# Performance work log

Measured on AMD Instinct MI355X. Metric: run time of the kernel, lower is better.

Reference implementation:

```python
import jax, jax.numpy as jnp
import numpy as np

H = 8  # num_heads

def layernorm(x, g, b, eps=1e-5):
    mu = jnp.mean(x, axis=-1, keepdims=True)
    var = jnp.var(x, axis=-1, keepdims=True)
    return (x - mu) * jax.lax.rsqrt(var + eps) * g + b

def mha(x, w_in, b_in, w_out, b_out, bias=None):
    # x: [B_, S, D]; w_in: [3D, D] packed q,k,v (PyTorch MHA layout)
    B_, S, D = x.shape
    hd = D // H
    qkv = x @ w_in.T + b_in                      # [B_, S, 3D]
    q, k, v = jnp.split(qkv, 3, axis=-1)
    def heads(t):
        return t.reshape(B_, S, H, hd).transpose(0, 2, 1, 3)  # [B_, H, S, hd]
    q, k, v = heads(q), heads(k), heads(v)
    scores = jnp.einsum('bhqd,bhkd->bhqk', q, k) / jnp.sqrt(jnp.float32(hd))
    if bias is not None:
        scores = scores + bias[None, None]        # broadcast [S,S] bias
    attn = jax.nn.softmax(scores, axis=-1)
    out = jnp.einsum('bhqk,bhkd->bhqd', attn, v)  # [B_, H, S, hd]
    out = out.transpose(0, 2, 1, 3).reshape(B_, S, D)
    return out @ w_out.T + b_out

def setup_inputs() -> dict:
    key = jax.random.key(0)
    ks = jax.random.split(key, 8)
    B, T, N, D, F = 32, 12, 325, 128, 512
    s = 0.05
    return {
        'x': jax.random.normal(ks[0], (B, T, N, D), jnp.float32),
        't_w_in': jax.random.normal(ks[1], (3 * D, D), jnp.float32) * s,
        't_b_in': jnp.zeros((3 * D,), jnp.float32),
        't_w_out': jax.random.normal(ks[2], (D, D), jnp.float32) * s,
        't_b_out': jnp.zeros((D,), jnp.float32),
        's_w_in': jax.random.normal(ks[3], (3 * D, D), jnp.float32) * s,
        's_b_in': jnp.zeros((3 * D,), jnp.float32),
        's_w_out': jax.random.normal(ks[4], (D, D), jnp.float32) * s,
        's_b_out': jnp.zeros((D,), jnp.float32),
        'g_bias': jax.random.normal(ks[5], (N, N), jnp.float32) * 0.5,
        'norm_t_g': jnp.ones((D,), jnp.float32),
        'norm_t_b': jnp.zeros((D,), jnp.float32),
        'norm_s_g': jnp.ones((D,), jnp.float32),
        'norm_s_b': jnp.zeros((D,), jnp.float32),
        'ff_w1': jax.random.normal(ks[6], (F, D), jnp.float32) * s,
        'ff_b1': jnp.zeros((F,), jnp.float32),
        'ff_w2': jax.random.normal(ks[7], (D, F), jnp.float32) * s,
        'ff_b2': jnp.zeros((D,), jnp.float32),
        'norm_ff_g': jnp.ones((D,), jnp.float32),
        'norm_ff_b': jnp.zeros((D,), jnp.float32),
    }

def reference(x, t_w_in, t_b_in, t_w_out, t_b_out, s_w_in, s_b_in, s_w_out, s_b_out,
              g_bias, norm_t_g, norm_t_b, norm_s_g, norm_s_b,
              ff_w1, ff_b1, ff_w2, ff_b2, norm_ff_g, norm_ff_b):
    B, T, N, D = x.shape
    # Temporal attention: each sensor attends over time
    xt = x.transpose(0, 2, 1, 3).reshape(B * N, T, D)
    xt = mha(xt, t_w_in, t_b_in, t_w_out, t_b_out)
    x = layernorm(x + xt.reshape(B, N, T, D).transpose(0, 2, 1, 3), norm_t_g, norm_t_b)
    # Spatial attention with graph bias: each timestep attends over sensors
    xs = x.reshape(B * T, N, D)
    xs = mha(xs, s_w_in, s_b_in, s_w_out, s_b_out, bias=g_bias)
    x = layernorm(x + xs.reshape(B, T, N, D), norm_s_g, norm_s_b)
    # FFN
    h = jax.nn.gelu(x @ ff_w1.T + ff_b1) @ ff_w2.T + ff_b2
    x = layernorm(x + h, norm_ff_g, norm_ff_b)
    return x
```

## Files before the change

kernel.cpp:

```cpp
#include <hip/hip_runtime.h>
#include <cstdint>
#include <cstddef>


#define B_ 32
#define T_ 12
#define N_ 325
#define D_ 128
#define H_ 8
#define F_ 512
#define NT 124800
#define BCH 8
#define CHK (BCH * T_ * N_)
#define NCHUNK 4
#define GT ((CHK + 63) / 64)
#define NKT 11
#define NQT 21
#define QSPLIT 3
#define QPG 7
#define GBS 328

#define O_XBF 0UL
#define O_Y1B 31948800UL
#define O_QKV 63897600UL
#define O_ABUF 87859200UL
#define O_WB 95846400UL
#define O_PB 96370688UL

typedef __attribute__((ext_vector_type(8))) short bf16x8;
typedef __attribute__((ext_vector_type(4))) short bf16x4;
typedef __attribute__((ext_vector_type(4))) float f32x4;

__device__ inline float b2f(unsigned short b) {
  unsigned int u = ((unsigned int)b) << 16;
  return __builtin_bit_cast(float, u);
}
__device__ inline unsigned short f2b(float f) {
  unsigned int u = __builtin_bit_cast(unsigned int, f);
  unsigned int r = (u + 0x7FFFu + ((u >> 16) & 1u)) >> 16;
  return (unsigned short)r;
}
__device__ inline unsigned short f2b_fast(float f) {
  unsigned int u = __builtin_bit_cast(unsigned int, f);
  return (unsigned short)((u + 0x8000u) >> 16);
}
__device__ inline f32x4 mfma16(bf16x8 a, bf16x8 b, f32x4 c) {
  return __builtin_amdgcn_mfma_f32_16x16x32_bf16(a, b, c, 0, 0, 0);
}
#if __has_builtin(__builtin_amdgcn_mfma_f32_16x16x16bf16_1k)
__device__ inline f32x4 mfma16k16(bf16x4 a, bf16x4 b, f32x4 c) {
  return __builtin_amdgcn_mfma_f32_16x16x16bf16_1k(a, b, c, 0, 0, 0);
}
#else
__device__ inline f32x4 mfma16k16(bf16x4 a, bf16x4 b, f32x4 c) {
  f32x4 d;
  asm volatile("s_nop 3\n\t"
               "v_mfma_f32_16x16x16_bf16 %0, %1, %2, %3\n\t"
               "s_nop 7\n\ts_nop 7"
               : "=&v"(d)
               : "v"(a), "v"(b), "v"(c));
  return d;
}
#endif
__device__ inline float gelu_t(float x) {
  float x3 = x * x * x;
  return 0.5f * x * (1.0f + tanhf(0.7978845608f * (x + 0.044715f * x3)));
}

__global__ void k_convert8(const void* __restrict__ src,
                           unsigned short* __restrict__ dB, long n8,
                           const unsigned short* __restrict__ probe) {
  long i = (long)blockIdx.x * blockDim.x + threadIdx.x;
  if (i >= n8) return;
  if (probe[0] != 0) {
    ((uint4*)dB)[i] = ((const uint4*)src)[i];
  } else {
    float4 a = ((const float4*)src)[i * 2];
    float4 b = ((const float4*)src)[i * 2 + 1];
    uint4 o;
    unsigned short* op = (unsigned short*)&o;
    op[0] = f2b(a.x); op[1] = f2b(a.y); op[2] = f2b(a.z); op[3] = f2b(a.w);
    op[4] = f2b(b.x); op[5] = f2b(b.y); op[6] = f2b(b.z); op[7] = f2b(b.w);
    ((uint4*)dB)[i] = o;
  }
}

__global__ void k_conv_params(
    const void* s1, const void* s2, const void* s3, const void* s4,
    const void* s5, const void* s6, const void* s7, const void* s8,
    const void* s9, const void* s10, const void* s11, const void* s12,
    const void* s13, const void* s14, const void* s15, const void* s16,
    const void* s17, const void* s18, const void* s19, char* ws,
    const unsigned short* __restrict__ probe) {
  long i = (long)blockIdx.x * blockDim.x + threadIdx.x;
  bool isbf = probe[0] != 0;
  long o = 0;
#define LOADV(src, j) \
  (isbf ? b2f(((const unsigned short*)(src))[j]) : ((const float*)(src))[j])
#define SEGB(src, dstoff, n)                                        \
  if (i < o + (n)) {                                                \
    long j = i - o;                                                 \
    ((unsigned short*)(ws + (dstoff)))[j] = f2b(LOADV(src, j));     \
    return;                                                         \
  }                                                                 \
  o += (n);
#define SEGF(src, dstoff, n)                              \
  if (i < o + (n)) {                                      \
    long j = i - o;                                       \
    ((float*)(ws + (dstoff)))[j] = LOADV(src, j);         \
    return;                                               \
  }                                                       \
  o += (n);
  SEGB(s1, O_WB + 0, 49152)
  SEGF(s2, O_PB + 0, 384)
  SEGB(s3, O_WB + 98304, 16384)
  SEGF(s4, O_PB + 1536, 128)
  SEGB(s5, O_WB + 131072, 49152)
  SEGF(s6, O_PB + 2048, 384)
  SEGB(s7, O_WB + 229376, 16384)
  SEGF(s8, O_PB + 3584, 128)
  if (i < o + 326 * GBS) {
    long j = i - o;
    int q = (int)(j / GBS);
    int s = (int)(j - (long)q * GBS);
    float v = (q < 325 && s < 325) ? LOADV(s9, (long)q * 325 + s) : 0.0f;
    ((float*)(ws + O_PB + 9728))[j] = v;
    return;
  }
  o += 326 * GBS;
  SEGF(s10, O_PB + 6656, 128)
  SEGF(s11, O_PB + 7168, 128)
  SEGF(s12, O_PB + 7680, 128)
  SEGF(s13, O_PB + 8192, 128)
  SEGB(s14, O_WB + 262144, 65536)
  SEGF(s15, O_PB + 4096, 512)
  SEGB(s16, O_WB + 393216, 65536)
  SEGF(s17, O_PB + 6144, 128)
  SEGF(s18, O_PB + 8704, 128)
  SEGF(s19, O_PB + 9216, 128)
#undef SEGB
#undef SEGF
#undef LOADV
}
#define CONVP_TOTAL 371504L

template <int ROWS, int KTOT>
__device__ inline void stage_tile(short (*dst)[ROWS][32],
                                  const unsigned short* __restrict__ src,
                                  int row0, int k0, int tid, int Mrows) {
  constexpr int CH = ROWS * 16;
#pragma unroll
  for (int it = 0; it < CH / 256; ++it) {
    int cb = tid + it * 256;
    int row = cb >> 4;
    int kc = cb & 15;
    int gr = row0 + row;
    gr = gr < Mrows ? gr : Mrows - 1;
    uint4 v = *(const uint4*)(src + (size_t)gr * KTOT + (size_t)k0 + kc * 8);
    *(uint4*)(&dst[kc >> 2][row][(kc & 3) * 8]) = v;
  }
}

template <int KTOT, bool GELU>
__global__ __launch_bounds__(256) void k_gemm_store(
    const unsigned short* __restrict__ Ab, const unsigned short* __restrict__ Wb,
    const float* __restrict__ bias, unsigned short* __restrict__ outB, int Ntot,
    int Mrows, int Nrows) {
  __shared__ __align__(16) union USm {
    struct { short A[4][64][32]; short B[4][64][32]; } s;
    float C[64][68];
  } sm;
  const int tid = threadIdx.x;
  const int m0 = blockIdx.x * 64;
  const int n0 = blockIdx.y * 64;
  const int lane = tid & 63, wave = tid >> 6;
  const int wm = wave >> 1, wn = wave & 1;
  const int ml = lane & 15, quad = lane >> 4;
  f32x4 acc[2][2] = {};
#pragma unroll
  for (int c = 0; c < KTOT / 128; ++c) {
    if (c) __syncthreads();
    stage_tile<64, KTOT>(sm.s.A, Ab, m0, c * 128, tid, Mrows);
    stage_tile<64, KTOT>(sm.s.B, Wb, n0, c * 128, tid, Nrows);
    __syncthreads();
#pragma unroll
    for (int kc = 0; kc < 4; ++kc) {
      bf16x8 a0 = *(const bf16x8*)&sm.s.A[kc][wm * 32 + ml][quad * 8];
      bf16x8 a1 = *(const bf16x8*)&sm.s.A[kc][wm * 32 + 16 + ml][quad * 8];
      bf16x8 b0 = *(const bf16x8*)&sm.s.B[kc][wn * 32 + ml][quad * 8];
      bf16x8 b1 = *(const bf16x8*)&sm.s.B[kc][wn * 32 + 16 + ml][quad * 8];
      acc[0][0] = mfma16(a0, b0, acc[0][0]);
      acc[0][1] = mfma16(a0, b1, acc[0][1]);
      acc[1][0] = mfma16(a1, b0, acc[1][0]);
      acc[1][1] = mfma16(a1, b1, acc[1][1]);
    }
  }
  __syncthreads();
#pragma unroll
  for (int mi = 0; mi < 2; ++mi)
#pragma unroll
    for (int ni = 0; ni < 2; ++ni)
#pragma unroll
      for (int r = 0; r < 4; ++r)
        sm.C[wm * 32 + mi * 16 + quad * 4 + r][wn * 32 + ni * 16 + ml] =
            acc[mi][ni][r];
  __syncthreads();
  const int trow = tid >> 4;
  const int tcol = (tid & 15) * 4;
  const float4 bv = *(const float4*)&bias[n0 + tcol];
#pragma unroll
  for (int it = 0; it < 4; ++it) {
    int row = it * 16 + trow;
    int gm = m0 + row;
    float4 cv = *(const float4*)&sm.C[row][tcol];
    float v0 = cv.x + bv.x, v1 = cv.y + bv.y, v2 = cv.z + bv.z,
          v3 = cv.w + bv.w;
    if (GELU) {
      v0 = gelu_t(v0); v1 = gelu_t(v1); v2 = gelu_t(v2); v3 = gelu_t(v3);
    }
    if (gm < Mrows) {
      ushort4 ov;
      ov.x = f2b(v0); ov.y = f2b(v1); ov.z = f2b(v2); ov.w = f2b(v3);
      *(ushort4*)&outB[(size_t)gm * Ntot + n0 + tcol] = ov;
    }
  }
}

template <int KTOT, bool FINAL>
__global__ __launch_bounds__(256) void k_gemm_ln(
    const unsigned short* __restrict__ Ab, const unsigned short* __restrict__ Wb,
    const float* __restrict__ bias, const unsigned short* __restrict__ resid,
    const float* __restrict__ gamma, const float* __restrict__ beta,
    unsigned short* __restrict__ outB, void* __restrict__ dOut, size_t row0g,
    const unsigned short* __restrict__ probe, int Mrows) {
  __shared__ __align__(16) union USm {
    struct { short A[4][64][32]; short B[4][128][32]; } s;
    float C[64][132];
  } sm;
  const int tid = threadIdx.x;
  const int m0 = blockIdx.x * 64;
  const int lane = tid & 63, wave = tid >> 6;
  const int wm = wave >> 1, wn = wave & 1;
  const int ml = lane & 15, quad = lane >> 4;
  f32x4 acc[2][4] = {};
#pragma unroll
  for (int c = 0; c < KTOT / 128; ++c) {
    if (c) __syncthreads();
    stage_tile<64, KTOT>(sm.s.A, Ab, m0, c * 128, tid, Mrows);
    stage_tile<128, KTOT>(sm.s.B, Wb, 0, c * 128, tid, 128);
    __syncthreads();
#pragma unroll
    for (int kc = 0; kc < 4; ++kc) {
      bf16x8 a[2], b[4];
#pragma unroll
      for (int mi = 0; mi < 2; ++mi)
        a[mi] = *(const bf16x8*)&sm.s.A[kc][wm * 32 + mi * 16 + ml][quad * 8];
#pragma unroll
      for (int ni = 0; ni < 4; ++ni)
        b[ni] = *(const bf16x8*)&sm.s.B[kc][wn * 64 + ni * 16 + ml][quad * 8];
#pragma unroll
      for (int mi = 0; mi < 2; ++mi)
#pragma unroll
        for (int ni = 0; ni < 4; ++ni)
          acc[mi][ni] = mfma16(a[mi], b[ni], acc[mi][ni]);
    }
  }
  __syncthreads();
#pragma unroll
  for (int mi = 0; mi < 2; ++mi)
#pragma unroll
    for (int ni = 0; ni < 4; ++ni)
#pragma unroll
      for (int r = 0; r < 4; ++r)
        sm.C[wm * 32 + mi * 16 + quad * 4 + r][wn * 64 + ni * 16 + ml] =
            acc[mi][ni][r];
  __syncthreads();
  const int c0 = lane * 2;
  const float bia0 = bias[c0], bia1 = bias[c0 + 1];
  const float ga0 = gamma[c0], ga1 = gamma[c0 + 1];
  const float be0 = beta[c0], be1 = beta[c0 + 1];
  const bool isbf = FINAL ? (probe[0] != 0) : true;
#pragma unroll
  for (int rr = 0; rr < 16; ++rr) {
    int row = wave * 16 + rr;
    int gm = m0 + row;
    bool valid = gm < Mrows;
    float2 cc = *(const float2*)&sm.C[row][c0];
    float r0 = 0.f, r1 = 0.f;
    if (valid) {
      ushort2 rv = *(const ushort2*)&resid[(size_t)gm * 128 + c0];
      r0 = b2f(rv.x);
      r1 = b2f(rv.y);
    }
    float v0 = cc.x + bia0 + r0, v1 = cc.y + bia1 + r1;
    float s = v0 + v1, q = v0 * v0 + v1 * v1;
#pragma unroll
    for (int off = 1; off < 64; off <<= 1) {
      s += __shfl_xor(s, off);
      q += __shfl_xor(q, off);
    }
    float mean = s * (1.f / 128.f);
    float var = q * (1.f / 128.f) - mean * mean;
    float rs = rsqrtf(var + 1e-5f);
    float y0 = (v0 - mean) * rs * ga0 + be0;
    float y1 = (v1 - mean) * rs * ga1 + be1;
    if (valid) {
      if (FINAL) {
        if (isbf) {
          ushort2 ov; ov.x = f2b(y0); ov.y = f2b(y1);
          *(ushort2*)((unsigned short*)dOut + (row0g + gm) * 128 + c0) = ov;
        } else {
          float2 ov; ov.x = y0; ov.y = y1;
          *(float2*)((float*)dOut + (row0g + gm) * 128 + c0) = ov;
        }
      } else {
        ushort2 ov; ov.x = f2b(y0); ov.y = f2b(y1);
        *(ushort2*)&outB[(size_t)gm * 128 + c0] = ov;
      }
    }
  }
}

__global__ __launch_bounds__(128) void k_attn_t(
    const unsigned short* __restrict__ qkv, unsigned short* __restrict__ A) {
  __shared__ float ls[12][384];
  const int tid = threadIdx.x;
  const int bx = blockIdx.x;
  const int b = bx / N_, n = bx % N_;
  for (int i = tid; i < 576; i += 128) {
    int t = i / 48, c = (i % 48) * 8;
    size_t tok = (size_t)(b * T_ + t) * N_ + n;
    uint4 v = *(const uint4*)(qkv + tok * 384 + c);
    const unsigned short* pv = (const unsigned short*)&v;
    float4 f0 = {b2f(pv[0]), b2f(pv[1]), b2f(pv[2]), b2f(pv[3])};
    float4 f1 = {b2f(pv[4]), b2f(pv[5]), b2f(pv[6]), b2f(pv[7])};
    *(float4*)&ls[t][c] = f0;
    *(float4*)&ls[t][c + 4] = f1;
  }
  __syncthreads();
  if (tid < 96) {
    int h = tid / 12, q = tid % 12;
    const float* qv = &ls[q][h * 16];
    float s[12];
    float m = -1e30f;
#pragma unroll
    for (int t = 0; t < 12; ++t) {
      float d = 0.f;
#pragma unroll
      for (int dd = 0; dd < 16; ++dd) d += qv[dd] * ls[t][128 + h * 16 + dd];
      s[t] = d * 0.25f;
      m = fmaxf(m, s[t]);
    }
    float l = 0.f;
#pragma unroll
    for (int t = 0; t < 12; ++t) {
      s[t] = __expf(s[t] - m);
      l += s[t];
    }
    float inv = 1.0f / l;
    float o[16];
#pragma unroll
    for (int dd = 0; dd < 16; ++dd) {
      float acc = 0.f;
#pragma unroll
      for (int t = 0; t < 12; ++t) acc += s[t] * ls[t][256 + h * 16 + dd];
      o[dd] = acc * inv;
    }
    size_t otok = (size_t)(b * T_ + q) * N_ + n;
#pragma unroll
    for (int g = 0; g < 4; ++g) {
      ushort4 ov;
      ov.x = f2b(o[g * 4 + 0]); ov.y = f2b(o[g * 4 + 1]);
      ov.z = f2b(o[g * 4 + 2]); ov.w = f2b(o[g * 4 + 3]);
      *(ushort4*)&A[otok * 128 + h * 16 + g * 4] = ov;
    }
  }
}

__global__ __launch_bounds__(256) void k_attn_s(
    const unsigned short* __restrict__ qkv, const float* __restrict__ gbp,
    unsigned short* __restrict__ A) {
  __shared__ short Ks[352 * 24];
  __shared__ short Vt[16 * 364];
  __shared__ uint4 zq;
  const int tid = threadIdx.x;
  const int bt = blockIdx.x, h = blockIdx.y, qs = blockIdx.z;
  const size_t base = (size_t)bt * N_;
  for (int i = tid; i < 352 * 2; i += 256) {
    int s = i >> 1, half = i & 1;
    if (s < N_) {
      size_t rb = (base + s) * 384 + h * 16 + half * 8;
      uint4 kv = *(const uint4*)(qkv + rb + 128);
      *(uint4*)&Ks[s * 24 + half * 8] = kv;
      uint4 vv = *(const uint4*)(qkv + rb + 256);
      const unsigned short* vs = (const unsigned short*)&vv;
#pragma unroll
      for (int e = 0; e < 8; ++e) Vt[(half * 8 + e) * 364 + s] = vs[e];
    } else {
      *(uint4*)&Ks[s * 24 + half * 8] = uint4{0, 0, 0, 0};
#pragma unroll
      for (int e = 0; e < 8; ++e) Vt[(half * 8 + e) * 364 + s] = 0;
    }
  }
  if (tid == 0) zq = uint4{0, 0, 0, 0};
  __syncthreads();
  const int lane = tid & 63, wave = tid >> 6;
  const int ml = lane & 15, quad = lane >> 4;
  const f32x4 fz = {0.f, 0.f, 0.f, 0.f};
  const int qt0 = qs * QPG, qt1 = qt0 + QPG;
  for (int qt = qt0 + wave; qt < qt1; qt += 4) {
    int q = qt * 16 + ml;
    int qc = q < N_ ? q : N_ - 1;
    bf16x8 qfrag = {0, 0, 0, 0, 0, 0, 0, 0};
    if (quad < 2)
      qfrag = *(const bf16x8*)(qkv + (base + qc) * 384 + h * 16 + quad * 8);
    const float* gb = gbp + (size_t)qc * GBS;
    f32x4 O = fz;
    float lsum = 0.f;
    for (int kt = 0; kt < NKT; ++kt) {
      const int sb = kt * 32;
      const short* kp0 =
          (quad < 2) ? &Ks[(sb + ml) * 24 + quad * 8] : (const short*)&zq;
      const short* kp1 =
          (quad < 2) ? &Ks[(sb + 16 + ml) * 24 + quad * 8] : (const short*)&zq;
      bf16x8 kf0 = *(const bf16x8*)kp0;
      bf16x8 kf1 = *(const bf16x8*)kp1;
      f32x4 S0 = mfma16(kf0, qfrag, fz);
      f32x4 S1 = mfma16(kf1, qfrag, fz);
      float4 g0 = *(const float4*)&gb[sb + quad * 4];
      const int sb1 = (sb + 16 <= 312) ? sb + 16 : 312;
      float4 g1 = *(const float4*)&gb[sb1 + quad * 4];
      float p0[4], p1[4];
      p0[0] = __expf(S0[0] * 0.25f + g0.x);
      p0[1] = __expf(S0[1] * 0.25f + g0.y);
      p0[2] = __expf(S0[2] * 0.25f + g0.z);
      p0[3] = __expf(S0[3] * 0.25f + g0.w);
      p1[0] = __expf(S1[0] * 0.25f + g1.x);
      p1[1] = __expf(S1[1] * 0.25f + g1.y);
      p1[2] = __expf(S1[2] * 0.25f + g1.z);
      p1[3] = __expf(S1[3] * 0.25f + g1.w);
      if (kt == NKT - 1) {
#pragma unroll
        for (int r = 0; r < 4; ++r) {
          if (sb + quad * 4 + r >= N_) p0[r] = 0.f;
          p1[r] = 0.f;
        }
      }
      lsum += p0[0] + p0[1] + p0[2] + p0[3] + p1[0] + p1[1] + p1[2] + p1[3];
      bf16x4 a0 = {(short)f2b_fast(p0[0]), (short)f2b_fast(p0[1]),
                   (short)f2b_fast(p0[2]), (short)f2b_fast(p0[3])};
      bf16x4 a1 = {(short)f2b_fast(p1[0]), (short)f2b_fast(p1[1]),
                   (short)f2b_fast(p1[2]), (short)f2b_fast(p1[3])};
      bf16x4 v0 = *(const bf16x4*)&Vt[ml * 364 + sb + quad * 4];
      bf16x4 v1 = *(const bf16x4*)&Vt[ml * 364 + sb + 16 + quad * 4];
      O = mfma16k16(a0, v0, O);
      O = mfma16k16(a1, v1, O);
    }
    lsum += __shfl_xor(lsum, 16);
    lsum += __shfl_xor(lsum, 32);
#pragma unroll
    for (int r = 0; r < 4; ++r) {
      int qg = qt * 16 + quad * 4 + r;
      float sr = __shfl(lsum, quad * 4 + r);
      if (qg < N_)
        A[(base + qg) * 128 + h * 16 + ml] = f2b(O[r] * (1.f / sr));
    }
  }
}

extern "C" void kernel_launch(void* const* d_in, const int* in_sizes, int n_in,
                              void* d_out, int out_size, void* d_ws,
                              size_t ws_size, hipStream_t stream) {
  char* ws = (char*)d_ws;
  const unsigned short* probe = (const unsigned short*)d_in[10];

  unsigned short* xbf = (unsigned short*)(ws + O_XBF);
  unsigned short* y1b = (unsigned short*)(ws + O_Y1B);
  unsigned short* qkvc = (unsigned short*)(ws + O_QKV);
  unsigned short* Abufc = (unsigned short*)(ws + O_ABUF);
  unsigned short* hbuf = qkvc;
  unsigned short* y2b = xbf;
  char* wb = ws + O_WB;
  unsigned short* wt_in = (unsigned short*)(wb + 0);
  unsigned short* wt_out = (unsigned short*)(wb + 98304);
  unsigned short* wsp_in = (unsigned short*)(wb + 131072);
  unsigned short* wsp_out = (unsigned short*)(wb + 229376);
  unsigned short* wff1 = (unsigned short*)(wb + 262144);
  unsigned short* wff2 = (unsigned short*)(wb + 393216);
  char* pb = ws + O_PB;
  float* p_t_b_in = (float*)(pb + 0);
  float* p_t_b_out = (float*)(pb + 1536);
  float* p_s_b_in = (float*)(pb + 2048);
  float* p_s_b_out = (float*)(pb + 3584);
  float* p_ff_b1 = (float*)(pb + 4096);
  float* p_ff_b2 = (float*)(pb + 6144);
  float* p_ntg = (float*)(pb + 6656);
  float* p_ntb = (float*)(pb + 7168);
  float* p_nsg = (float*)(pb + 7680);
  float* p_nsb = (float*)(pb + 8192);
  float* p_nfg = (float*)(pb + 8704);
  float* p_nfb = (float*)(pb + 9216);
  float* p_gbp = (float*)(pb + 9728);

  {
    long n8 = (long)NT * 128 / 8;
    k_convert8<<<dim3((unsigned)((n8 + 255) / 256)), dim3(256), 0, stream>>>(
        d_in[0], xbf, n8, probe);
    k_conv_params<<<dim3((unsigned)((CONVP_TOTAL + 255) / 256)), dim3(256), 0,
                    stream>>>(d_in[1], d_in[2], d_in[3], d_in[4], d_in[5],
                              d_in[6], d_in[7], d_in[8], d_in[9], d_in[10],
                              d_in[11], d_in[12], d_in[13], d_in[14], d_in[15],
                              d_in[16], d_in[17], d_in[18], d_in[19], ws,
                              probe);
  }

  dim3 blk(256);
  for (int c = 0; c < NCHUNK; ++c) {
    size_t tok0 = (size_t)c * CHK;
    k_gemm_store<128, false><<<dim3(GT, 6), blk, 0, stream>>>(
        xbf + tok0 * 128, wt_in, p_t_b_in, qkvc, 384, CHK, 384);
    k_attn_t<<<dim3(BCH * N_), dim3(128), 0, stream>>>(qkvc, Abufc);
    k_gemm_ln<128, false><<<dim3(GT), blk, 0, stream>>>(
        Abufc, wt_out, p_t_b_out, xbf + tok0 * 128, p_ntg, p_ntb,
        y1b + tok0 * 128, nullptr, 0, probe, CHK);
  }
  for (int c = 0; c < NCHUNK; ++c) {
    size_t tok0 = (size_t)c * CHK;
    k_gemm_store<128, false><<<dim3(GT, 6), blk, 0, stream>>>(
        y1b + tok0 * 128, wsp_in, p_s_b_in, qkvc, 384, CHK, 384);
    k_attn_s<<<dim3(BCH * T_, H_, QSPLIT), blk, 0, stream>>>(qkvc, p_gbp,
                                                             Abufc);
    k_gemm_ln<128, false><<<dim3(GT), blk, 0, stream>>>(
        Abufc, wsp_out, p_s_b_out, y1b + tok0 * 128, p_nsg, p_nsb,
        y2b + tok0 * 128, nullptr, 0, probe, CHK);
  }
  for (int c = 0; c < NCHUNK; ++c) {
    size_t tok0 = (size_t)c * CHK;
    k_gemm_store<128, true><<<dim3(GT, 8), blk, 0, stream>>>(
        y2b + tok0 * 128, wff1, p_ff_b1, hbuf, 512, CHK, 512);
    k_gemm_ln<512, true><<<dim3(GT), blk, 0, stream>>>(
        hbuf, wff2, p_ff_b2, y2b + tok0 * 128, p_nfg, p_nfb, nullptr, d_out,
        tok0, probe, CHK);
  }
}
```

Before: 726.5 us.

## Restructure spatial attention: two q-tiles per wave, exp2, MFMA row sums

Each wave in the spatial attention kernel now processes two query tiles together, sharing K and V fragment loads between them. QK^T uses the 16x16x16 MFMA with 4-element fragments instead of the zero-padded 32-deep one. The log2(e) factor is folded into the precomputed graph bias and the score scale, so the exponent becomes a single fma plus exp2. Softmax row sums come from an MFMA against a ones vector instead of scalar adds and shuffles. The costs are higher register pressure and row sums computed from bf16-rounded probabilities.

```diff
diff --git a/kernel.cpp b/kernel.cpp
--- a/kernel.cpp
+++ b/kernel.cpp
@@ -30,6 +30,16 @@
 typedef __attribute__((ext_vector_type(8))) short bf16x8;
 typedef __attribute__((ext_vector_type(4))) short bf16x4;
 typedef __attribute__((ext_vector_type(4))) float f32x4;
+typedef __attribute__((ext_vector_type(2))) unsigned int u32x2;
+typedef __attribute__((ext_vector_type(4))) unsigned int u32x4;
+
+#define SCL 0.36067376022224085f
+
+#if __has_builtin(__builtin_amdgcn_exp2f)
+#define EXP2(x) __builtin_amdgcn_exp2f(x)
+#else
+#define EXP2(x) __expf((x) * 0.6931471805599453f)
+#endif
 
 __device__ inline float b2f(unsigned short b) {
   unsigned int u = ((unsigned int)b) << 16;
@@ -62,6 +72,12 @@
   return d;
 }
 #endif
+__device__ inline bf16x8 cat44(bf16x4 a, bf16x4 b) {
+  u32x2 ua = __builtin_bit_cast(u32x2, a);
+  u32x2 ub = __builtin_bit_cast(u32x2, b);
+  u32x4 u = {ua.x, ua.y, ub.x, ub.y};
+  return __builtin_bit_cast(bf16x8, u);
+}
 __device__ inline float gelu_t(float x) {
   float x3 = x * x * x;
   return 0.5f * x * (1.0f + tanhf(0.7978845608f * (x + 0.044715f * x3)));
@@ -123,7 +139,8 @@
     long j = i - o;
     int q = (int)(j / GBS);
     int s = (int)(j - (long)q * GBS);
-    float v = (q < 325 && s < 325) ? LOADV(s9, (long)q * 325 + s) : 0.0f;
+    float v = (q < 325 && s < 325) ? LOADV(s9, (long)q * 325 + s) * 1.44269504f
+                                   : 0.0f;
     ((float*)(ws + O_PB + 9728))[j] = v;
     return;
   }
@@ -382,7 +399,6 @@
     unsigned short* __restrict__ A) {
   __shared__ short Ks[352 * 24];
   __shared__ short Vt[16 * 364];
-  __shared__ uint4 zq;
   const int tid = threadIdx.x;
   const int bt = blockIdx.x, h = blockIdx.y, qs = blockIdx.z;
   const size_t base = (size_t)bt * N_;
@@ -402,68 +418,87 @@
       for (int e = 0; e < 8; ++e) Vt[(half * 8 + e) * 364 + s] = 0;
     }
   }
-  if (tid == 0) zq = uint4{0, 0, 0, 0};
   __syncthreads();
   const int lane = tid & 63, wave = tid >> 6;
   const int ml = lane & 15, quad = lane >> 4;
   const f32x4 fz = {0.f, 0.f, 0.f, 0.f};
-  const int qt0 = qs * QPG, qt1 = qt0 + QPG;
-  for (int qt = qt0 + wave; qt < qt1; qt += 4) {
-    int q = qt * 16 + ml;
-    int qc = q < N_ ? q : N_ - 1;
-    bf16x8 qfrag = {0, 0, 0, 0, 0, 0, 0, 0};
-    if (quad < 2)
-      qfrag = *(const bf16x8*)(qkv + (base + qc) * 384 + h * 16 + quad * 8);
-    const float* gb = gbp + (size_t)qc * GBS;
-    f32x4 O = fz;
-    float lsum = 0.f;
-    for (int kt = 0; kt < NKT; ++kt) {
-      const int sb = kt * 32;
-      const short* kp0 =
-          (quad < 2) ? &Ks[(sb + ml) * 24 + quad * 8] : (const short*)&zq;
-      const short* kp1 =
-          (quad < 2) ? &Ks[(sb + 16 + ml) * 24 + quad * 8] : (const short*)&zq;
-      bf16x8 kf0 = *(const bf16x8*)kp0;
-      bf16x8 kf1 = *(const bf16x8*)kp1;
-      f32x4 S0 = mfma16(kf0, qfrag, fz);
-      f32x4 S1 = mfma16(kf1, qfrag, fz);
-      float4 g0 = *(const float4*)&gb[sb + quad * 4];
-      const int sb1 = (sb + 16 <= 312) ? sb + 16 : 312;
-      float4 g1 = *(const float4*)&gb[sb1 + quad * 4];
-      float p0[4], p1[4];
-      p0[0] = __expf(S0[0] * 0.25f + g0.x);
-      p0[1] = __expf(S0[1] * 0.25f + g0.y);
-      p0[2] = __expf(S0[2] * 0.25f + g0.z);
-      p0[3] = __expf(S0[3] * 0.25f + g0.w);
-      p1[0] = __expf(S1[0] * 0.25f + g1.x);
-      p1[1] = __expf(S1[1] * 0.25f + g1.y);
-      p1[2] = __expf(S1[2] * 0.25f + g1.z);
-      p1[3] = __expf(S1[3] * 0.25f + g1.w);
-      if (kt == NKT - 1) {
-#pragma unroll
-        for (int r = 0; r < 4; ++r) {
-          if (sb + quad * 4 + r >= N_) p0[r] = 0.f;
-          p1[r] = 0.f;
-        }
+  const bf16x8 ones8 = {16256, 16256, 16256, 16256,
+                        16256, 16256, 16256, 16256};
+  const int qt0 = qs * QPG;
+  const int qtA = qt0 + wave;
+  const bool hasB = wave < 3;
+  const int qtB = hasB ? qtA + 4 : qtA;
+  const int qA = qtA * 16 + ml, qB = qtB * 16 + ml;
+  const int qcA = qA < N_ ? qA : N_ - 1;
+  const int qcB = qB < N_ ? qB : N_ - 1;
+  const bf16x4 qfA =
+      *(const bf16x4*)(qkv + (base + qcA) * 384 + h * 16 + quad * 4);
+  const bf16x4 qfB =
+      *(const bf16x4*)(qkv + (base + qcB) * 384 + h * 16 + quad * 4);
+  const float* gbA = gbp + (size_t)qcA * GBS;
+  const float* gbB = gbp + (size_t)qcB * GBS;
+  f32x4 OA = fz, OB = fz, LA = fz, LB = fz;
+  for (int kt = 0; kt < NKT; ++kt) {
+    const int sb = kt * 32;
+    bf16x4 k0f = *(const bf16x4*)&Ks[(sb + ml) * 24 + quad * 4];
+    bf16x4 k1f = *(const bf16x4*)&Ks[(sb + 16 + ml) * 24 + quad * 4];
+    f32x4 S0A = mfma16k16(k0f, qfA, fz);
+    f32x4 S1A = mfma16k16(k1f, qfA, fz);
+    f32x4 S0B = mfma16k16(k0f, qfB, fz);
+    f32x4 S1B = mfma16k16(k1f, qfB, fz);
+    const int sb1 = (sb + 16 <= 312) ? sb + 16 : 312;
+    float4 g0A = *(const float4*)&gbA[sb + quad * 4];
+    float4 g1A = *(const float4*)&gbA[sb1 + quad * 4];
+    float4 g0B = *(const float4*)&gbB[sb + quad * 4];
+    float4 g1B = *(const float4*)&gbB[sb1 + quad * 4];
+    float p0A[4], p1A[4], p0B[4], p1B[4];
+#define EXPV(p, S, g)                      \
+  p[0] = EXP2(fmaf(S[0], SCL, g.x));       \
+  p[1] = EXP2(fmaf(S[1], SCL, g.y));       \
+  p[2] = EXP2(fmaf(S[2], SCL, g.z));       \
+  p[3] = EXP2(fmaf(S[3], SCL, g.w));
+    EXPV(p0A, S0A, g0A)
+    EXPV(p1A, S1A, g1A)
+    EXPV(p0B, S0B, g0B)
+    EXPV(p1B, S1B, g1B)
+#undef EXPV
+    if (kt == NKT - 1) {
+#pragma unroll
+      for (int r = 0; r < 4; ++r) {
+        if (sb + quad * 4 + r >= N_) { p0A[r] = 0.f; p0B[r] = 0.f; }
+        p1A[r] = 0.f;
+        p1B[r] = 0.f;
       }
-      lsum += p0[0] + p0[1] + p0[2] + p0[3] + p1[0] + p1[1] + p1[2] + p1[3];
-      bf16x4 a0 = {(short)f2b_fast(p0[0]), (short)f2b_fast(p0[1]),
-                   (short)f2b_fast(p0[2]), (short)f2b_fast(p0[3])};
-      bf16x4 a1 = {(short)f2b_fast(p1[0]), (short)f2b_fast(p1[1]),
-                   (short)f2b_fast(p1[2]), (short)f2b_fast(p1[3])};
-      bf16x4 v0 = *(const bf16x4*)&Vt[ml * 364 + sb + quad * 4];
-      bf16x4 v1 = *(const bf16x4*)&Vt[ml * 364 + sb + 16 + quad * 4];
-      O = mfma16k16(a0, v0, O);
-      O = mfma16k16(a1, v1, O);
-    }
-    lsum += __shfl_xor(lsum, 16);
-    lsum += __shfl_xor(lsum, 32);
+    }
+    bf16x4 a0A = {(short)f2b_fast(p0A[0]), (short)f2b_fast(p0A[1]),
+                  (short)f2b_fast(p0A[2]), (short)f2b_fast(p0A[3])};
+    bf16x4 a1A = {(short)f2b_fast(p1A[0]), (short)f2b_fast(p1A[1]),
+                  (short)f2b_fast(p1A[2]), (short)f2b_fast(p1A[3])};
+    bf16x4 a0B = {(short)f2b_fast(p0B[0]), (short)f2b_fast(p0B[1]),
+                  (short)f2b_fast(p0B[2]), (short)f2b_fast(p0B[3])};
+    bf16x4 a1B = {(short)f2b_fast(p1B[0]), (short)f2b_fast(p1B[1]),
+                  (short)f2b_fast(p1B[2]), (short)f2b_fast(p1B[3])};
+    bf16x4 v0 = *(const bf16x4*)&Vt[ml * 364 + sb + quad * 4];
+    bf16x4 v1 = *(const bf16x4*)&Vt[ml * 364 + sb + 16 + quad * 4];
+    OA = mfma16k16(a0A, v0, OA);
+    OA = mfma16k16(a1A, v1, OA);
+    OB = mfma16k16(a0B, v0, OB);
+    OB = mfma16k16(a1B, v1, OB);
+    LA = mfma16(cat44(a0A, a1A), ones8, LA);
+    LB = mfma16(cat44(a0B, a1B), ones8, LB);
+  }
+#pragma unroll
+  for (int r = 0; r < 4; ++r) {
+    int qg = qtA * 16 + quad * 4 + r;
+    if (qg < N_)
+      A[(base + qg) * 128 + h * 16 + ml] = f2b(OA[r] / LA[r]);
+  }
+  if (hasB) {
 #pragma unroll
     for (int r = 0; r < 4; ++r) {
-      int qg = qt * 16 + quad * 4 + r;
-      float sr = __shfl(lsum, quad * 4 + r);
+      int qg = qtB * 16 + quad * 4 + r;
       if (qg < N_)
-        A[(base + qg) * 128 + h * 16 + ml] = f2b(O[r] * (1.f / sr));
+        A[(base + qg) * 128 + h * 16 + ml] = f2b(OB[r] / LB[r]);
     }
   }
 }
```

Measured after the change: 731.7 us. No clear change (+0.7%).
